# Performance work log

Measured on AMD Instinct MI355X. Metric: run time of the kernel, lower is better.

## Reference

```python
import jax, jax.numpy as jnp
import numpy as np

CUTOFF = 0.05

def _freq_filter(x_chw, filter_type):
    # x_chw: [C,H,W] = batch element 0, detached in the original (stop_gradient)
    x = jax.lax.stop_gradient(x_chw)
    C, H, W = x.shape
    a = jnp.abs(x)
    mn = a.min(axis=(1, 2), keepdims=True)
    ptp = a.max(axis=(1, 2), keepdims=True) - mn
    # np.uint8(255*(a-mn)/ptp): values in [0,255], cast truncates -> floor
    q = jnp.floor(255.0 * (a - mn) / ptp)
    f = jnp.fft.fftshift(jnp.fft.fft2(q), axes=(-2, -1))
    crow, ccol = H // 2, W // 2
    dr, dc = int(CUTOFF * crow), int(CUTOFF * ccol)
    m = jnp.zeros((H, W), dtype=q.dtype)
    m = m.at[crow - dr:crow + dr, ccol - dc:ccol + dc].set(1.0)
    if filter_type == 'low_pass':
        m = 1.0 - m  # note: original 'low_pass' actually removes low freqs
    out = jnp.abs(jnp.fft.ifft2(jnp.fft.ifftshift(f * m, axes=(-2, -1))))
    return out.astype(x_chw.dtype)  # [C,H,W]

def _conv1x1(x, w, b):
    # x: [B,C,H,W], w: [O,C], b: [O]
    return jnp.einsum('oc,bchw->bohw', w, x) + b[None, :, None, None]

def setup_inputs() -> dict:
    key = jax.random.key(0)
    ks = jax.random.split(key, 7)
    B, C, H, W = 1, 256, 96, 96
    fuse = jax.random.normal(ks[0], (B, C, H, W), dtype=jnp.float32)
    s = 1.0 / np.sqrt(C)
    Wq = jax.random.normal(ks[1], (C, C), dtype=jnp.float32) * s
    bq = jax.random.normal(ks[2], (C,), dtype=jnp.float32) * 0.01
    Wk = jax.random.normal(ks[3], (C, C), dtype=jnp.float32) * s
    bk = jax.random.normal(ks[4], (C,), dtype=jnp.float32) * 0.01
    Wv = jax.random.normal(ks[5], (C, C), dtype=jnp.float32) * s
    bv = jax.random.normal(ks[6], (C,), dtype=jnp.float32) * 0.01
    return {"fuse": fuse, "Wq": Wq, "bq": bq, "Wk": Wk, "bk": bk, "Wv": Wv, "bv": bv}

def reference(fuse, Wq, bq, Wk, bk, Wv, bv):
    B, C, H, W = fuse.shape
    scale = 1.0 / (C ** 0.5)
    # frequency-filtered maps (computed from batch 0, broadcast to all batches)
    FQ = jnp.broadcast_to(_freq_filter(fuse[0], 'high_pass'), fuse.shape)
    FK = jnp.broadcast_to(_freq_filter(fuse[0], 'low_pass'), fuse.shape)
    fuse_Query = _conv1x1(FQ, Wq, bq).reshape(B, C, H * W)     # [B,C,HW]
    fuse_Q_mask = fuse_Query.reshape(B * H, C * W)             # [B*H, C*W]
    fuse_Query_t = jnp.transpose(fuse_Query, (0, 2, 1))        # [B,HW,C]
    fuse_Key = _conv1x1(FK, Wk, bk).reshape(B, C, H * W)       # [B,C,HW]
    Fuse_Q_mask = jnp.max(fuse_Q_mask, axis=0, keepdims=True)  # [1, C*W]
    mask_KQ = jnp.einsum('bnc,bcm->bnm', fuse_Query_t, fuse_Key) * scale  # [B,HW,HW]
    mask_KQ = jax.nn.softmax(mask_KQ, axis=0)  # softmax over batch dim (as in original)
    mask_KQ = jnp.max(mask_KQ, axis=1)                         # [B,HW]
    mask_KQ = mask_KQ.reshape(-1, W)                           # [B*H, W]
    mask_KQ = jnp.max(mask_KQ, axis=-1, keepdims=True)         # [B*H, 1]
    mask = (mask_KQ @ Fuse_Q_mask).reshape(B, C, H, W)
    fuse_Value = _conv1x1(fuse, Wv, bv)
    return fuse_Value + fuse_Value * mask
```

## Files before the change

### kernel.cpp

```cpp
#include <hip/hip_runtime.h>
#include <math.h>

#define CCH 256
#define HW  9216
#define CW  24576
#define TWO_PI 6.28318530717958647692f

typedef __attribute__((ext_vector_type(8))) short short8;
typedef __attribute__((ext_vector_type(4))) float f32x4;

__device__ inline unsigned short f2bf(float f) {
    unsigned u = __float_as_uint(f);
    unsigned r = (u + 0x7FFFu + ((u >> 16) & 1u)) >> 16;
    return (unsigned short)r;
}

__global__ __launch_bounds__(768) void k_pre(const float* __restrict__ x,
                                             const float* __restrict__ Wq,
                                             const float* __restrict__ Wv,
                                             short8* __restrict__ Wqt,
                                             short8* __restrict__ Wvt,
                                             unsigned* __restrict__ FQm,
                                             float* __restrict__ Fg) {
    __shared__ float qa[HW];
    __shared__ float cs[96][2];
    __shared__ float Gp[8][96][5];
    __shared__ float Gs[96][6];
    __shared__ float red[24];
    __shared__ float s_mn, s_ptp;
    int bid = blockIdx.x, t = threadIdx.x;

    if (bid >= 256) {
        int widx = bid - 256;
        if (t < 256) {
            const float* src = (widx >= 32) ? Wv : Wq;
            short8* dst = (widx >= 32) ? Wvt : Wqt;
            int cidx = (widx & 31) * 256 + t;
            int ot = cidx >> 11, kc = (cidx >> 6) & 31, m = cidx & 63;
            const float* s = src + (ot * 64 + m) * 256 + kc * 8;
            short8 v;
            #pragma unroll
            for (int e = 0; e < 8; ++e) v[e] = (short)f2bf(s[e]);
            dst[cidx] = v;
        }
        return;
    }

    int c = bid;
    if (t < 96) FQm[c * 96 + t] = 0u;
    const float* xp = x + c * HW;
    if (t < 96) { float a = TWO_PI * (float)t / 96.0f; cs[t][0] = cosf(a); cs[t][1] = sinf(a); }
    float lo = 1e30f, hi = 0.f;
    #pragma unroll
    for (int i = 0; i < 12; ++i) {
        float a = fabsf(xp[t + i * 768]);
        qa[t + i * 768] = a;
        lo = fminf(lo, a);
        hi = fmaxf(hi, a);
    }
    #pragma unroll
    for (int d = 32; d; d >>= 1) {
        lo = fminf(lo, __shfl_xor(lo, d, 64));
        hi = fmaxf(hi, __shfl_xor(hi, d, 64));
    }
    if ((t & 63) == 0) { red[t >> 6] = lo; red[12 + (t >> 6)] = hi; }
    __syncthreads();
    if (t == 0) {
        lo = red[0]; hi = red[12];
        #pragma unroll
        for (int i = 1; i < 12; ++i) { lo = fminf(lo, red[i]); hi = fmaxf(hi, red[12 + i]); }
        s_mn = lo; s_ptp = hi - lo;
    }
    __syncthreads();
    float mn = s_mn, ptp = s_ptp;

    {
        int xx = t % 96, h = t / 96;
        float g0r = 0, g0i = 0, g1r = 0, g1i = 0, g2 = 0;
        for (int y = h * 12; y < h * 12 + 12; ++y) {
            float q = floorf(255.0f * (qa[y * 96 + xx] - mn) / ptp);
            float c1 = cs[y][0], s1 = cs[y][1];
            float c2 = c1 * c1 - s1 * s1, s2 = 2.0f * c1 * s1;
            g0r += q * c2; g0i += q * s2;
            g1r += q * c1; g1i += q * s1;
            g2  += q;
        }
        Gp[h][xx][0] = g0r; Gp[h][xx][1] = g0i;
        Gp[h][xx][2] = g1r; Gp[h][xx][3] = g1i;
        Gp[h][xx][4] = g2;
    }
    __syncthreads();
    if (t < 96) {
        #pragma unroll
        for (int j = 0; j < 5; ++j) {
            float s = 0.f;
            #pragma unroll
            for (int h = 0; h < 8; ++h) s += Gp[h][t][j];
            Gs[t][j] = s;
        }
        Gs[t][5] = 0.f;
    }
    __syncthreads();
    if (t < 64) {
        int coef = t >> 2, qq = t & 3;
        int ky = coef >> 2, kx = coef & 3;
        float fr = 0, fi = 0;
        for (int xx = qq * 24; xx < qq * 24 + 24; ++xx) {
            float c1 = cs[xx][0], s1 = cs[xx][1];
            float er, ei;
            if (kx == 0)      { er = c1 * c1 - s1 * s1; ei = 2.0f * c1 * s1; }
            else if (kx == 1) { er = c1; ei = s1; }
            else if (kx == 2) { er = 1.f; ei = 0.f; }
            else              { er = c1; ei = -s1; }
            float gr, gi;
            if (ky == 0)      { gr = Gs[xx][0]; gi = Gs[xx][1]; }
            else if (ky == 1) { gr = Gs[xx][2]; gi = Gs[xx][3]; }
            else if (ky == 2) { gr = Gs[xx][4]; gi = 0.f; }
            else              { gr = Gs[xx][2]; gi = -Gs[xx][3]; }
            fr += gr * er - gi * ei;
            fi += gr * ei + gi * er;
        }
        fr += __shfl_xor(fr, 1, 64); fr += __shfl_xor(fr, 2, 64);
        fi += __shfl_xor(fi, 1, 64); fi += __shfl_xor(fi, 2, 64);
        if (qq == 0) {
            Fg[c * 32 + 2 * coef]     = fr;
            Fg[c * 32 + 2 * coef + 1] = fi;
        }
    }
}

__global__ __launch_bounds__(256) void k_gemmQV(const short8* __restrict__ Wqt,
                                                const short8* __restrict__ Wvt,
                                                const float* __restrict__ Fg,
                                                const float* __restrict__ bq,
                                                const float* __restrict__ bv,
                                                const float* __restrict__ x,
                                                unsigned* __restrict__ FQm,
                                                float* __restrict__ out) {
    __shared__ short8 As[2048];
    __shared__ short8 Bs[2048];
    __shared__ float Rs[2048][2];
    int tid = threadIdx.x;
    int pt_ = blockIdx.x;
    bool isQ = blockIdx.y < 4;
    int ot = isQ ? blockIdx.y : blockIdx.y - 4;
    const short8* wsrc = (isQ ? Wqt : Wvt) + ot * 2048;
    #pragma unroll
    for (int i = 0; i < 8; ++i) As[i * 256 + tid] = wsrc[i * 256 + tid];

    int p0 = pt_ * 64;
    if (isQ) {
        int y0 = p0 / 96;
        {
            int yi = (tid >> 2) & 1, kx = tid & 3, cb = tid >> 3;
            float ay = TWO_PI * (float)(y0 + yi) / 96.0f;
            float cyv = cosf(ay), syv = sinf(ay);
            float cy2 = cyv * cyv - syv * syv, sy2 = 2.f * cyv * syv;
            float Ur[4] = { cy2, cyv, 1.f, cyv };
            float Ui[4] = { -sy2, -syv, 0.f, syv };
            #pragma unroll
            for (int i = 0; i < 8; ++i) {
                int cc = cb + i * 32;
                float rr = 0.f, ri = 0.f;
                #pragma unroll
                for (int ky = 0; ky < 4; ++ky) {
                    float fr = Fg[cc * 32 + 2 * (ky * 4 + kx)];
                    float fi = Fg[cc * 32 + 2 * (ky * 4 + kx) + 1];
                    rr += fr * Ur[ky] - fi * Ui[ky];
                    ri += fr * Ui[ky] + fi * Ur[ky];
                }
                Rs[cc * 8 + yi * 4 + kx][0] = rr;
                Rs[cc * 8 + yi * 4 + kx][1] = ri;
            }
        }
        __syncthreads();
        const float inv = 1.0f / 9216.0f;
        #pragma unroll
        for (int i = 0; i < 8; ++i) {
            int si = i * 256 + tid;
            int kcg = si >> 6, n = si & 63;
            int p = p0 + n;
            int y = p / 96, xx = p - y * 96;
            int yi = y - y0;
            float axv = TWO_PI * (float)xx / 96.0f;
            float cxv = cosf(axv), sxv = sinf(axv);
            float cx2 = cxv * cxv - sxv * sxv, sx2 = 2.f * cxv * sxv;
            float Tr[4] = { cx2, cxv, 1.f, cxv };
            float Ti[4] = { -sx2, -sxv, 0.f, sxv };
            short8 vv;
            #pragma unroll
            for (int e = 0; e < 8; ++e) {
                int rb = (kcg * 8 + e) * 8 + yi * 4;
                float ar = 0.f, ai = 0.f;
                #pragma unroll
                for (int kx = 0; kx < 4; ++kx) {
                    float rr = Rs[rb + kx][0], ri = Rs[rb + kx][1];
                    ar += rr * Tr[kx] - ri * Ti[kx];
                    ai += rr * Ti[kx] + ri * Tr[kx];
                }
                vv[e] = (short)f2bf(sqrtf(ar * ar + ai * ai) * inv);
            }
            Bs[si] = vv;
        }
    } else {
        #pragma unroll
        for (int i = 0; i < 8; ++i) {
            int si = i * 256 + tid;
            int KC = si >> 6, n = si & 63;
            const float* xb = x + (size_t)(KC * 8) * HW + p0 + n;
            short8 v;
            #pragma unroll
            for (int e = 0; e < 8; ++e) v[e] = (short)f2bf(xb[(size_t)e * HW]);
            Bs[si] = v;
        }
    }
    __syncthreads();

    int l = tid & 63, w = tid >> 6;
    int wr = w >> 1, wc = w & 1;
    int l15 = l & 15, quad = l >> 4;
    f32x4 acc[2][2] = {};
    int abase = wr * 32 + l15;
    int bbase = wc * 32 + l15;
    #pragma unroll
    for (int s = 0; s < 8; ++s) {
        int kc = s * 4 + quad;
        short8 a0 = As[kc * 64 + abase];
        short8 a1 = As[kc * 64 + abase + 16];
        short8 b0 = Bs[kc * 64 + bbase];
        short8 b1 = Bs[kc * 64 + bbase + 16];
        acc[0][0] = __builtin_amdgcn_mfma_f32_16x16x32_bf16(a0, b0, acc[0][0], 0, 0, 0);
        acc[0][1] = __builtin_amdgcn_mfma_f32_16x16x32_bf16(a0, b1, acc[0][1], 0, 0, 0);
        acc[1][0] = __builtin_amdgcn_mfma_f32_16x16x32_bf16(a1, b0, acc[1][0], 0, 0, 0);
        acc[1][1] = __builtin_amdgcn_mfma_f32_16x16x32_bf16(a1, b1, acc[1][1], 0, 0, 0);
    }

    if (isQ) {
        #pragma unroll
        for (int ni = 0; ni < 2; ++ni) {
            #pragma unroll
            for (int r = 0; r < 4; ++r) {
                int o_lo = ot * 64 + wr * 32 + quad * 4 + r;
                float v = fmaxf(acc[0][ni][r] + bq[o_lo], acc[1][ni][r] + bq[o_lo + 16]);
                v = fmaxf(v, __shfl_xor(v, 32, 64));
                if (quad < 2) {
                    int p = pt_ * 64 + wc * 32 + ni * 16 + l15;
                    int k = ((quad * 4 + r) & 7) * HW + p;
                    if (k >= CW) k -= CW;
                    if (k >= CW) k -= CW;
                    unsigned u = __float_as_uint(v);
                    unsigned key = (u & 0x80000000u) ? ~u : (u | 0x80000000u);
                    atomicMax(&FQm[k], key);
                }
            }
        }
    } else {
        #pragma unroll
        for (int mi = 0; mi < 2; ++mi) {
            #pragma unroll
            for (int ni = 0; ni < 2; ++ni) {
                #pragma unroll
                for (int r = 0; r < 4; ++r) {
                    int o = ot * 64 + wr * 32 + mi * 16 + quad * 4 + r;
                    int p = pt_ * 64 + wc * 32 + ni * 16 + l15;
                    out[(size_t)o * HW + p] = acc[mi][ni][r] + bv[o];
                }
            }
        }
    }
}

__device__ inline float mdecode(unsigned key) {
    unsigned ub = (key & 0x80000000u) ? (key ^ 0x80000000u) : ~key;
    return __uint_as_float(ub);
}
__global__ __launch_bounds__(256) void k_mask(float* __restrict__ out,
                                              const unsigned* __restrict__ FQm) {
    int i = (blockIdx.x * 256 + threadIdx.x) * 8;
    int o = i / HW;
    int p = i - o * HW;
    int k = (o & 7) * HW + p;
    if (k >= CW) k -= CW;
    if (k >= CW) k -= CW;
    float4 v0 = *(const float4*)(out + i);
    float4 v1 = *(const float4*)(out + i + 4);
    uint4 k0 = *(const uint4*)(FQm + k);
    uint4 k1 = *(const uint4*)(FQm + k + 4);
    v0.x *= 1.0f + mdecode(k0.x); v0.y *= 1.0f + mdecode(k0.y);
    v0.z *= 1.0f + mdecode(k0.z); v0.w *= 1.0f + mdecode(k0.w);
    v1.x *= 1.0f + mdecode(k1.x); v1.y *= 1.0f + mdecode(k1.y);
    v1.z *= 1.0f + mdecode(k1.z); v1.w *= 1.0f + mdecode(k1.w);
    *(float4*)(out + i)     = v0;
    *(float4*)(out + i + 4) = v1;
}

extern "C" void kernel_launch(void* const* d_in, const int* in_sizes, int n_in,
                              void* d_out, int out_size, void* d_ws, size_t ws_size,
                              hipStream_t stream) {
    const float* fuse = (const float*)d_in[0];
    const float* Wq   = (const float*)d_in[1];
    const float* bq   = (const float*)d_in[2];
    const float* Wv   = (const float*)d_in[5];
    const float* bv   = (const float*)d_in[6];
    float* out = (float*)d_out;

    char* ws = (char*)d_ws;
    unsigned* FQm = (unsigned*)(ws);
    float*    Fg  = (float*)(ws + 98304);
    short8*   Wqt = (short8*)(ws + 131072);
    short8*   Wvt = (short8*)(ws + 262144);

    k_pre<<<320, 768, 0, stream>>>(fuse, Wq, Wv, Wqt, Wvt, FQm, Fg);
    k_gemmQV<<<dim3(144, 8), 256, 0, stream>>>(Wqt, Wvt, Fg, bq, bv, fuse, FQm, out);
    k_mask<<<1152, 256, 0, stream>>>(out, FQm);
}
```

Baseline: 113.4 us.

## Split Q and V GEMMs and fuse mask multiply into V GEMM epilogue

The combined Q/V GEMM kernel is split into separate Q and V kernels. The V kernel now runs after the Q max-reduction finishes and applies the mask factor in its epilogue, so the separate elementwise mask pass is removed. This saves one full read and write of the output tensor. The cost is that Q and V work no longer run concurrently in one launch, which halves the grid of each GEMM.

```diff
diff --git a/kernel.cpp b/kernel.cpp
--- a/kernel.cpp
+++ b/kernel.cpp
@@ -129,90 +129,72 @@
     }
 }
 
-__global__ __launch_bounds__(256) void k_gemmQV(const short8* __restrict__ Wqt,
-                                                const short8* __restrict__ Wvt,
-                                                const float* __restrict__ Fg,
-                                                const float* __restrict__ bq,
-                                                const float* __restrict__ bv,
-                                                const float* __restrict__ x,
-                                                unsigned* __restrict__ FQm,
-                                                float* __restrict__ out) {
+__global__ __launch_bounds__(256) void k_gemmQ(const short8* __restrict__ Wqt,
+                                               const float* __restrict__ Fg,
+                                               const float* __restrict__ bq,
+                                               unsigned* __restrict__ FQm) {
     __shared__ short8 As[2048];
     __shared__ short8 Bs[2048];
     __shared__ float Rs[2048][2];
     int tid = threadIdx.x;
     int pt_ = blockIdx.x;
-    bool isQ = blockIdx.y < 4;
-    int ot = isQ ? blockIdx.y : blockIdx.y - 4;
-    const short8* wsrc = (isQ ? Wqt : Wvt) + ot * 2048;
+    int ot = blockIdx.y;
+    const short8* wsrc = Wqt + ot * 2048;
     #pragma unroll
     for (int i = 0; i < 8; ++i) As[i * 256 + tid] = wsrc[i * 256 + tid];
 
     int p0 = pt_ * 64;
-    if (isQ) {
-        int y0 = p0 / 96;
-        {
-            int yi = (tid >> 2) & 1, kx = tid & 3, cb = tid >> 3;
-            float ay = TWO_PI * (float)(y0 + yi) / 96.0f;
-            float cyv = cosf(ay), syv = sinf(ay);
-            float cy2 = cyv * cyv - syv * syv, sy2 = 2.f * cyv * syv;
-            float Ur[4] = { cy2, cyv, 1.f, cyv };
-            float Ui[4] = { -sy2, -syv, 0.f, syv };
-            #pragma unroll
-            for (int i = 0; i < 8; ++i) {
-                int cc = cb + i * 32;
-                float rr = 0.f, ri = 0.f;
-                #pragma unroll
-                for (int ky = 0; ky < 4; ++ky) {
-                    float fr = Fg[cc * 32 + 2 * (ky * 4 + kx)];
-                    float fi = Fg[cc * 32 + 2 * (ky * 4 + kx) + 1];
-                    rr += fr * Ur[ky] - fi * Ui[ky];
-                    ri += fr * Ui[ky] + fi * Ur[ky];
-                }
-                Rs[cc * 8 + yi * 4 + kx][0] = rr;
-                Rs[cc * 8 + yi * 4 + kx][1] = ri;
+    int y0 = p0 / 96;
+    {
+        int yi = (tid >> 2) & 1, kx = tid & 3, cb = tid >> 3;
+        float ay = TWO_PI * (float)(y0 + yi) / 96.0f;
+        float cyv = cosf(ay), syv = sinf(ay);
+        float cy2 = cyv * cyv - syv * syv, sy2 = 2.f * cyv * syv;
+        float Ur[4] = { cy2, cyv, 1.f, cyv };
+        float Ui[4] = { -sy2, -syv, 0.f, syv };
+        #pragma unroll
+        for (int i = 0; i < 8; ++i) {
+            int cc = cb + i * 32;
+            float rr = 0.f, ri = 0.f;
+            #pragma unroll
+            for (int ky = 0; ky < 4; ++ky) {
+                float fr = Fg[cc * 32 + 2 * (ky * 4 + kx)];
+                float fi = Fg[cc * 32 + 2 * (ky * 4 + kx) + 1];
+                rr += fr * Ur[ky] - fi * Ui[ky];
+                ri += fr * Ui[ky] + fi * Ur[ky];
             }
-        }
-        __syncthreads();
-        const float inv = 1.0f / 9216.0f;
-        #pragma unroll
-        for (int i = 0; i < 8; ++i) {
-            int si = i * 256 + tid;
-            int kcg = si >> 6, n = si & 63;
-            int p = p0 + n;
-            int y = p / 96, xx = p - y * 96;
-            int yi = y - y0;
-            float axv = TWO_PI * (float)xx / 96.0f;
-            float cxv = cosf(axv), sxv = sinf(axv);
-            float cx2 = cxv * cxv - sxv * sxv, sx2 = 2.f * cxv * sxv;
-            float Tr[4] = { cx2, cxv, 1.f, cxv };
-            float Ti[4] = { -sx2, -sxv, 0.f, sxv };
-            short8 vv;
-            #pragma unroll
-            for (int e = 0; e < 8; ++e) {
-                int rb = (kcg * 8 + e) * 8 + yi * 4;
-                float ar = 0.f, ai = 0.f;
-                #pragma unroll
-                for (int kx = 0; kx < 4; ++kx) {
-                    float rr = Rs[rb + kx][0], ri = Rs[rb + kx][1];
-                    ar += rr * Tr[kx] - ri * Ti[kx];
-                    ai += rr * Ti[kx] + ri * Tr[kx];
-                }
-                vv[e] = (short)f2bf(sqrtf(ar * ar + ai * ai) * inv);
+            Rs[cc * 8 + yi * 4 + kx][0] = rr;
+            Rs[cc * 8 + yi * 4 + kx][1] = ri;
+        }
+    }
+    __syncthreads();
+    const float inv = 1.0f / 9216.0f;
+    #pragma unroll
+    for (int i = 0; i < 8; ++i) {
+        int si = i * 256 + tid;
+        int kcg = si >> 6, n = si & 63;
+        int p = p0 + n;
+        int y = p / 96, xx = p - y * 96;
+        int yi = y - y0;
+        float axv = TWO_PI * (float)xx / 96.0f;
+        float cxv = cosf(axv), sxv = sinf(axv);
+        float cx2 = cxv * cxv - sxv * sxv, sx2 = 2.f * cxv * sxv;
+        float Tr[4] = { cx2, cxv, 1.f, cxv };
+        float Ti[4] = { -sx2, -sxv, 0.f, sxv };
+        short8 vv;
+        #pragma unroll
+        for (int e = 0; e < 8; ++e) {
+            int rb = (kcg * 8 + e) * 8 + yi * 4;
+            float ar = 0.f, ai = 0.f;
+            #pragma unroll
+            for (int kx = 0; kx < 4; ++kx) {
+                float rr = Rs[rb + kx][0], ri = Rs[rb + kx][1];
+                ar += rr * Tr[kx] - ri * Ti[kx];
+                ai += rr * Ti[kx] + ri * Tr[kx];
             }
-            Bs[si] = vv;
-        }
-    } else {
-        #pragma unroll
-        for (int i = 0; i < 8; ++i) {
-            int si = i * 256 + tid;
-            int KC = si >> 6, n = si & 63;
-            const float* xb = x + (size_t)(KC * 8) * HW + p0 + n;
-            short8 v;
-            #pragma unroll
-            for (int e = 0; e < 8; ++e) v[e] = (short)f2bf(xb[(size_t)e * HW]);
-            Bs[si] = v;
-        }
+            vv[e] = (short)f2bf(sqrtf(ar * ar + ai * ai) * inv);
+        }
+        Bs[si] = vv;
     }
     __syncthreads();
 
@@ -235,36 +217,21 @@
         acc[1][1] = __builtin_amdgcn_mfma_f32_16x16x32_bf16(a1, b1, acc[1][1], 0, 0, 0);
     }
 
-    if (isQ) {
-        #pragma unroll
-        for (int ni = 0; ni < 2; ++ni) {
-            #pragma unroll
-            for (int r = 0; r < 4; ++r) {
-                int o_lo = ot * 64 + wr * 32 + quad * 4 + r;
-                float v = fmaxf(acc[0][ni][r] + bq[o_lo], acc[1][ni][r] + bq[o_lo + 16]);
-                v = fmaxf(v, __shfl_xor(v, 32, 64));
-                if (quad < 2) {
-                    int p = pt_ * 64 + wc * 32 + ni * 16 + l15;
-                    int k = ((quad * 4 + r) & 7) * HW + p;
-                    if (k >= CW) k -= CW;
-                    if (k >= CW) k -= CW;
-                    unsigned u = __float_as_uint(v);
-                    unsigned key = (u & 0x80000000u) ? ~u : (u | 0x80000000u);
-                    atomicMax(&FQm[k], key);
-                }
-            }
-        }
-    } else {
-        #pragma unroll
-        for (int mi = 0; mi < 2; ++mi) {
-            #pragma unroll
-            for (int ni = 0; ni < 2; ++ni) {
-                #pragma unroll
-                for (int r = 0; r < 4; ++r) {
-                    int o = ot * 64 + wr * 32 + mi * 16 + quad * 4 + r;
-                    int p = pt_ * 64 + wc * 32 + ni * 16 + l15;
-                    out[(size_t)o * HW + p] = acc[mi][ni][r] + bv[o];
-                }
+    #pragma unroll
+    for (int ni = 0; ni < 2; ++ni) {
+        #pragma unroll
+        for (int r = 0; r < 4; ++r) {
+            int o_lo = ot * 64 + wr * 32 + quad * 4 + r;
+            float v = fmaxf(acc[0][ni][r] + bq[o_lo], acc[1][ni][r] + bq[o_lo + 16]);
+            v = fmaxf(v, __shfl_xor(v, 32, 64));
+            if (quad < 2) {
+                int p = pt_ * 64 + wc * 32 + ni * 16 + l15;
+                int k = ((quad * 4 + r) & 7) * HW + p;
+                if (k >= CW) k -= CW;
+                if (k >= CW) k -= CW;
+                unsigned u = __float_as_uint(v);
+                unsigned key = (u & 0x80000000u) ? ~u : (u | 0x80000000u);
+                atomicMax(&FQm[k], key);
             }
         }
     }
@@ -274,24 +241,68 @@
     unsigned ub = (key & 0x80000000u) ? (key ^ 0x80000000u) : ~key;
     return __uint_as_float(ub);
 }
-__global__ __launch_bounds__(256) void k_mask(float* __restrict__ out,
-                                              const unsigned* __restrict__ FQm) {
-    int i = (blockIdx.x * 256 + threadIdx.x) * 8;
-    int o = i / HW;
-    int p = i - o * HW;
-    int k = (o & 7) * HW + p;
-    if (k >= CW) k -= CW;
-    if (k >= CW) k -= CW;
-    float4 v0 = *(const float4*)(out + i);
-    float4 v1 = *(const float4*)(out + i + 4);
-    uint4 k0 = *(const uint4*)(FQm + k);
-    uint4 k1 = *(const uint4*)(FQm + k + 4);
-    v0.x *= 1.0f + mdecode(k0.x); v0.y *= 1.0f + mdecode(k0.y);
-    v0.z *= 1.0f + mdecode(k0.z); v0.w *= 1.0f + mdecode(k0.w);
-    v1.x *= 1.0f + mdecode(k1.x); v1.y *= 1.0f + mdecode(k1.y);
-    v1.z *= 1.0f + mdecode(k1.z); v1.w *= 1.0f + mdecode(k1.w);
-    *(float4*)(out + i)     = v0;
-    *(float4*)(out + i + 4) = v1;
+__global__ __launch_bounds__(256) void k_gemmV(const short8* __restrict__ Wvt,
+                                               const float* __restrict__ bv,
+                                               const float* __restrict__ x,
+                                               const unsigned* __restrict__ FQm,
+                                               float* __restrict__ out) {
+    __shared__ short8 As[2048];
+    __shared__ short8 Bs[2048];
+    int tid = threadIdx.x;
+    int pt_ = blockIdx.x;
+    int ot = blockIdx.y;
+    const short8* wsrc = Wvt + ot * 2048;
+    #pragma unroll
+    for (int i = 0; i < 8; ++i) As[i * 256 + tid] = wsrc[i * 256 + tid];
+
+    int p0 = pt_ * 64;
+    #pragma unroll
+    for (int i = 0; i < 8; ++i) {
+        int si = i * 256 + tid;
+        int KC = si >> 6, n = si & 63;
+        const float* xb = x + (size_t)(KC * 8) * HW + p0 + n;
+        short8 v;
+        #pragma unroll
+        for (int e = 0; e < 8; ++e) v[e] = (short)f2bf(xb[(size_t)e * HW]);
+        Bs[si] = v;
+    }
+    __syncthreads();
+
+    int l = tid & 63, w = tid >> 6;
+    int wr = w >> 1, wc = w & 1;
+    int l15 = l & 15, quad = l >> 4;
+    f32x4 acc[2][2] = {};
+    int abase = wr * 32 + l15;
+    int bbase = wc * 32 + l15;
+    #pragma unroll
+    for (int s = 0; s < 8; ++s) {
+        int kc = s * 4 + quad;
+        short8 a0 = As[kc * 64 + abase];
+        short8 a1 = As[kc * 64 + abase + 16];
+        short8 b0 = Bs[kc * 64 + bbase];
+        short8 b1 = Bs[kc * 64 + bbase + 16];
+        acc[0][0] = __builtin_amdgcn_mfma_f32_16x16x32_bf16(a0, b0, acc[0][0], 0, 0, 0);
+        acc[0][1] = __builtin_amdgcn_mfma_f32_16x16x32_bf16(a0, b1, acc[0][1], 0, 0, 0);
+        acc[1][0] = __builtin_amdgcn_mfma_f32_16x16x32_bf16(a1, b0, acc[1][0], 0, 0, 0);
+        acc[1][1] = __builtin_amdgcn_mfma_f32_16x16x32_bf16(a1, b1, acc[1][1], 0, 0, 0);
+    }
+
+    #pragma unroll
+    for (int mi = 0; mi < 2; ++mi) {
+        #pragma unroll
+        for (int ni = 0; ni < 2; ++ni) {
+            #pragma unroll
+            for (int r = 0; r < 4; ++r) {
+                int o = ot * 64 + wr * 32 + mi * 16 + quad * 4 + r;
+                int p = pt_ * 64 + wc * 32 + ni * 16 + l15;
+                int k = (o & 7) * HW + p;
+                if (k >= CW) k -= CW;
+                if (k >= CW) k -= CW;
+                float m = mdecode(FQm[k]);
+                out[(size_t)o * HW + p] = (acc[mi][ni][r] + bv[o]) * (1.0f + m);
+            }
+        }
+    }
 }
 
 extern "C" void kernel_launch(void* const* d_in, const int* in_sizes, int n_in,
@@ -311,6 +322,6 @@
     short8*   Wvt = (short8*)(ws + 262144);
 
     k_pre<<<320, 768, 0, stream>>>(fuse, Wq, Wv, Wqt, Wvt, FQm, Fg);
-    k_gemmQV<<<dim3(144, 8), 256, 0, stream>>>(Wqt, Wvt, Fg, bq, bv, fuse, FQm, out);
-    k_mask<<<1152, 256, 0, stream>>>(out, FQm);
-}
+    k_gemmQ<<<dim3(144, 4), 256, 0, stream>>>(Wqt, Fg, bq, FQm);
+    k_gemmV<<<dim3(144, 4), 256, 0, stream>>>(Wvt, bv, fuse, FQm, out);
+}
```

Result: no change. 114.8 us (+1.2%).
